# Kernel optimization log

Hardware: AMD Instinct MI355X
Metric: run time of the kernel (lower is better)

Reference implementation:

```python
import jax, jax.numpy as jnp
import numpy as np

N_HEAD = 16


def setup_inputs() -> dict:
    key = jax.random.key(0)
    ks = jax.random.split(key, 10)
    N, C, P = 4096, 2048, 8
    s = lambda k, shape, scale: jax.random.normal(k, shape, dtype=jnp.float32) * scale
    return {
        "x": s(ks[0], (N, C), 1.0),
        "rwkv_state": s(ks[1], (N, C), 1.0),
        "Wq": s(ks[2], (C, C), C ** -0.5),
        "Wk": s(ks[3], (C, C), C ** -0.5),
        "Wv": s(ks[4], (C, C), C ** -0.5),
        "Wo": s(ks[5], (C, C), 0.1 * C ** -0.5),
        "Wg": s(ks[6], (C, C), C ** -0.5),
        "bg": jnp.zeros((C,), dtype=jnp.float32),
        "Wb": s(ks[7], (2 * C, P * C), (2 * C) ** -0.5),
        "Wr": s(ks[8], (C, C), C ** -0.5),
    }


def reference(x, rwkv_state, Wq, Wk, Wv, Wo, Wg, bg, Wb, Wr):
    N, C = x.shape
    H = N_HEAD
    D = C // H
    # bridge: produce per-token tiny prefix [N, P, C] + reconstruction loss
    xs = jnp.concatenate([x, rwkv_state], axis=-1)      # [N, 2C]
    prefix = (xs @ Wb).reshape(N, -1, C)                # [N, P, C]
    recon = prefix.mean(axis=1) @ Wr                    # [N, C]
    recon_loss = jnp.mean((recon - x) ** 2)
    # per-token attention: query length 1 over P prefix keys
    q = (x @ Wq).reshape(N, H, D)                       # [N, H, D]
    k = (prefix @ Wk).reshape(N, -1, H, D)              # [N, P, H, D]
    v = (prefix @ Wv).reshape(N, -1, H, D)
    scores = jnp.einsum('nhd,nphd->nhp', q, k) / jnp.sqrt(jnp.float32(D))
    attn = jax.nn.softmax(scores, axis=-1)              # [N, H, P]
    out = jnp.einsum('nhp,nphd->nhd', attn, v).reshape(N, C)
    g = jax.nn.sigmoid(x @ Wg + bg)
    out = (out @ Wo) * g
    return out, recon_loss
```

## Files before the change

### kernel.cpp

```cpp
#include <hip/hip_runtime.h>

#define DEVFN static __device__ __forceinline__

typedef __attribute__((ext_vector_type(8))) short short8;
typedef __attribute__((ext_vector_type(4))) float f32x4;

DEVFN unsigned short f2bf(float f) {
    union { float f; unsigned u; } a; a.f = f;
    unsigned u = a.u;
    unsigned r = (u + 0x7FFFu + ((u >> 16) & 1u)) >> 16;
    return (unsigned short)r;
}
DEVFN float bf2f(unsigned short b) {
    union { unsigned u; float f; } a; a.u = ((unsigned)b) << 16;
    return a.f;
}
DEVFN float2 bfpair(unsigned v) {
    float2 r;
    union { unsigned u; float f; } a;
    a.u = (v & 0xFFFFu) << 16; r.x = a.f;
    a.u = v & 0xFFFF0000u;     r.y = a.f;
    return r;
}

DEVFN void gload16(const void* g, void* lds) {
    __builtin_amdgcn_global_load_lds(
        (const __attribute__((address_space(1))) unsigned int*)g,
        (__attribute__((address_space(3))) unsigned int*)lds, 16, 0, 0);
}

#define BAR() __builtin_amdgcn_s_barrier()
#define VMCNT8() asm volatile("s_waitcnt vmcnt(8)" ::: "memory")
#define VMCNT0() asm volatile("s_waitcnt vmcnt(0)" ::: "memory")

__global__ __launch_bounds__(256) void pack_xs_kernel(
        const float* __restrict__ x, const float* __restrict__ r,
        unsigned short* __restrict__ xs) {
    int i = blockIdx.x * 256 + threadIdx.x;
    int n  = i >> 10;
    int cw = i & 1023;
    const float* src = (cw < 512) ? (x + (size_t)n * 2048 + cw * 4)
                                  : (r + (size_t)n * 2048 + (cw - 512) * 4);
    float4 v = *(const float4*)src;
    ushort4 o;
    o.x = f2bf(v.x); o.y = f2bf(v.y); o.z = f2bf(v.z); o.w = f2bf(v.w);
    *(ushort4*)(xs + (size_t)n * 4096 + cw * 4) = o;
}

DEVFN void transpose_body(const float* __restrict__ in,
                          unsigned short* __restrict__ out,
                          int R, int Cc, int bx, int by) {
    __shared__ float tile[32][33];
    const int t  = threadIdx.x;
    const int r  = t >> 3;
    const int c4 = (t & 7) * 4;
    const int tr = by * 32, tc = bx * 32;
    float4 v = *(const float4*)(in + (size_t)(tr + r) * Cc + tc + c4);
    tile[r][c4 + 0] = v.x; tile[r][c4 + 1] = v.y;
    tile[r][c4 + 2] = v.z; tile[r][c4 + 3] = v.w;
    __syncthreads();
    const int orow = r, oc = c4;
    ushort4 o;
    o.x = f2bf(tile[oc + 0][orow]);
    o.y = f2bf(tile[oc + 1][orow]);
    o.z = f2bf(tile[oc + 2][orow]);
    o.w = f2bf(tile[oc + 3][orow]);
    *(ushort4*)(out + (size_t)(tc + orow) * R + tr + oc) = o;
}

__global__ __launch_bounds__(256) void transpose_cast_kernel(
        const float* __restrict__ in, unsigned short* __restrict__ out,
        int R, int Cc) {
    transpose_body(in, out, R, Cc, blockIdx.x, blockIdx.y);
}

__global__ __launch_bounds__(256) void transpose_cast6_kernel(
        const float* __restrict__ i0, const float* __restrict__ i1,
        const float* __restrict__ i2, const float* __restrict__ i3,
        const float* __restrict__ i4, const float* __restrict__ i5,
        unsigned short* __restrict__ o0, unsigned short* __restrict__ o1,
        unsigned short* __restrict__ o2, unsigned short* __restrict__ o3,
        unsigned short* __restrict__ o4, unsigned short* __restrict__ o5) {
    const float* in; unsigned short* out;
    switch (blockIdx.z) {
        case 0: in = i0; out = o0; break;
        case 1: in = i1; out = o1; break;
        case 2: in = i2; out = o2; break;
        case 3: in = i3; out = o3; break;
        case 4: in = i4; out = o4; break;
        default: in = i5; out = o5; break;
    }
    transpose_body(in, out, 2048, 2048, blockIdx.x, blockIdx.y);
}

template <int EPI>
__global__ __launch_bounds__(512, 2) void gemm256(
        const unsigned short* __restrict__ A, int lda,
        const unsigned short* __restrict__ Bt, int ldb,
        void* __restrict__ Cptr, void* __restrict__ Cptr2,
        int ldc, int splitcol, int K, int Mtiles,
        const float* __restrict__ aux_f32,
        const unsigned short* __restrict__ aux_bf16,
        float* __restrict__ loss_accum,
        const unsigned short* __restrict__ A2,
        const unsigned short* __restrict__ Bt2) {
    extern __shared__ char smem[];
    const int tid  = threadIdx.x;
    const int wid  = tid >> 6, lane = tid & 63;
    const int wm   = wid >> 2, wn = wid & 3;
    const int l15  = lane & 15;
    const int lhi  = (lane >> 4) * 16;
    const int nkt  = K >> 6;

    int bid = blockIdx.x;
    bool sub1 = false;
    if constexpr (EPI == 5) {
        const int half = gridDim.x >> 1;
        if (bid >= half) { sub1 = true; bid -= half; A = A2; Bt = Bt2; }
    }

    const int bandH = Mtiles >> 3;
    const int xcd = bid & 7, idx = bid >> 3;
    const int brow = (xcd * bandH + (idx % bandH)) << 8;
    const int bcol = (idx / bandH) << 8;

    const int lin0 = (wid * 2 + 0) * 1024 + lane * 16;
    const int lin1 = (wid * 2 + 1) * 1024 + lane * 16;
    const int ph0 = lin0 ^ (((lin0 >> 7) & 7) << 4);
    const int ph1v = lin1 ^ (((lin1 >> 7) & 7) << 4);
    const int srow0 = ph0 >> 7, scol0 = (ph0 & 127) >> 1;
    const int srow1 = ph1v >> 7, scol1 = (ph1v & 127) >> 1;
    const int dst0 = (wid * 2 + 0) * 1024;
    const int dst1 = (wid * 2 + 1) * 1024;

#define STAGE(t, mat, h) do { \
        char* base_ = smem + (((t) & 1) * 65536) + ((mat) * 32768) + ((h) * 16384); \
        const unsigned short* G_ = (mat) ? Bt : A; \
        const int ld_ = (mat) ? ldb : lda; \
        const int rb_ = ((mat) ? bcol : brow) + (h) * 128; \
        gload16(G_ + (size_t)(rb_ + srow0) * ld_ + (t) * 64 + scol0, base_ + dst0); \
        gload16(G_ + (size_t)(rb_ + srow1) * ld_ + (t) * 64 + scol1, base_ + dst1); \
    } while (0)
#define STAGE_G(t, mat, h) do { if ((t) < nkt) STAGE(t, mat, h); } while (0)

#define LDA_FRAG(dst, buf, m, kk) do { \
        int lin_ = ((m) * 16 + l15) * 128 + (kk) * 64 + lhi; \
        int ph_  = lin_ ^ (((lin_ >> 7) & 7) << 4); \
        dst = *(const short8*)(smem + (buf) * 65536 + wm * 16384 + ph_); \
    } while (0)
#define LDB_FRAG(dst, buf, n, kk) do { \
        int lin_ = ((wn & 1) * 64 + (n) * 16 + l15) * 128 + (kk) * 64 + lhi; \
        int ph_  = lin_ ^ (((lin_ >> 7) & 7) << 4); \
        dst = *(const short8*)(smem + (buf) * 65536 + 32768 + (wn >> 1) * 16384 + ph_); \
    } while (0)

    f32x4 acc[8][4] = {};
    short8 afr[8][2], bfr[4][2];

#define MFMA_Q(mq) do { \
        __builtin_amdgcn_s_setprio(1); \
        _Pragma("unroll") \
        for (int n_ = 0; n_ < 4; ++n_) { \
            acc[2*(mq)][n_]   = __builtin_amdgcn_mfma_f32_16x16x32_bf16(afr[2*(mq)][0],   bfr[n_][0], acc[2*(mq)][n_],   0,0,0); \
            acc[2*(mq)][n_]   = __builtin_amdgcn_mfma_f32_16x16x32_bf16(afr[2*(mq)][1],   bfr[n_][1], acc[2*(mq)][n_],   0,0,0); \
            acc[2*(mq)+1][n_] = __builtin_amdgcn_mfma_f32_16x16x32_bf16(afr[2*(mq)+1][0], bfr[n_][0], acc[2*(mq)+1][n_], 0,0,0); \
            acc[2*(mq)+1][n_] = __builtin_amdgcn_mfma_f32_16x16x32_bf16(afr[2*(mq)+1][1], bfr[n_][1], acc[2*(mq)+1][n_], 0,0,0); \
        } \
        __builtin_amdgcn_s_setprio(0); \
    } while (0)

#define READ_B(b) do { \
        _Pragma("unroll") \
        for (int n_ = 0; n_ < 4; ++n_) { LDB_FRAG(bfr[n_][0], b, n_, 0); LDB_FRAG(bfr[n_][1], b, n_, 1); } \
    } while (0)
#define READ_QA(b, mq) do { \
        LDA_FRAG(afr[2*(mq)][0],   b, 2*(mq),   0); LDA_FRAG(afr[2*(mq)][1],   b, 2*(mq),   1); \
        LDA_FRAG(afr[2*(mq)+1][0], b, 2*(mq)+1, 0); LDA_FRAG(afr[2*(mq)+1][1], b, 2*(mq)+1, 1); \
    } while (0)

    STAGE(0, 1, 0); STAGE(0, 1, 1); STAGE(0, 0, 0); STAGE(0, 0, 1);
    STAGE_G(1, 1, 0); STAGE_G(1, 1, 1); STAGE_G(1, 0, 0); STAGE_G(1, 0, 1);
    VMCNT8();
    BAR();

    const int niter = nkt >> 1;
    for (int it = 0; it < niter; ++it) {
        const int t0 = it * 2, t1 = t0 + 1;
        const bool lastIt = (it == niter - 1);

        READ_B(0); READ_QA(0, 0);
        BAR();
        MFMA_Q(0);
        READ_QA(0, 1);
        STAGE_G(t0 + 2, 1, 0);
        BAR();
        MFMA_Q(1);
        READ_QA(0, 2); READ_QA(0, 3);
        STAGE_G(t0 + 2, 1, 1);
        BAR();
        MFMA_Q(2);
        STAGE_G(t0 + 2, 0, 0); STAGE_G(t0 + 2, 0, 1);
        if (lastIt) { VMCNT0(); } else { VMCNT8(); }
        BAR();
        MFMA_Q(3);

        READ_B(1); READ_QA(1, 0);
        BAR();
        MFMA_Q(0);
        READ_QA(1, 1);
        STAGE_G(t1 + 2, 1, 0);
        BAR();
        MFMA_Q(1);
        READ_QA(1, 2); READ_QA(1, 3);
        STAGE_G(t1 + 2, 1, 1);
        BAR();
        MFMA_Q(2);
        STAGE_G(t1 + 2, 0, 0); STAGE_G(t1 + 2, 0, 1);
        if (lastIt) { VMCNT0(); } else { VMCNT8(); }
        BAR();
        MFMA_Q(3);
    }

    const int rl = (lane >> 4) * 4;
    const int cl = lane & 15;
    const int row0 = brow + wm * 128;

    if constexpr (EPI == 5) {
        const int col0 = bcol + wn * 64;
        if (!sub1) {
            float lsum = 0.f;
#pragma unroll
            for (int m = 0; m < 8; m++)
#pragma unroll
                for (int n = 0; n < 4; n++)
#pragma unroll
                    for (int rg = 0; rg < 4; rg++) {
                        int gr = row0 + m * 16 + rl + rg;
                        int gc = col0 + n * 16 + cl;
                        float d = acc[m][n][rg] - aux_f32[(size_t)gr * ldc + gc];
                        lsum += d * d;
                    }
#pragma unroll
            for (int msk = 1; msk < 64; msk <<= 1)
                lsum += __shfl_xor(lsum, msk, 64);
            if (lane == 0) atomicAdd(loss_accum, lsum);
        } else {
#pragma unroll
            for (int m = 0; m < 8; m++)
#pragma unroll
                for (int n = 0; n < 4; n++)
#pragma unroll
                    for (int rg = 0; rg < 4; rg++) {
                        int gr = row0 + m * 16 + rl + rg;
                        int gc = col0 + n * 16 + cl;
                        size_t idxo = (size_t)gr * ldc + gc;
                        float gv = bf2f(aux_bf16[idxo]);
                        ((float*)Cptr)[idxo] = acc[m][n][rg] * gv;
                    }
        }
        return;
    }

    void* Ceff = Cptr;
    bool second = false;
    int bcol_l = bcol;
    if constexpr (EPI == 0 || EPI == 4) {
        if (bcol >= splitcol) { Ceff = Cptr2; bcol_l = bcol - splitcol; second = true; }
    }
    const int col0 = bcol_l + wn * 64;

#pragma unroll
    for (int m = 0; m < 8; m++)
#pragma unroll
        for (int n = 0; n < 4; n++)
#pragma unroll
            for (int rg = 0; rg < 4; rg++) {
                int gr = row0 + m * 16 + rl + rg;
                int gc = col0 + n * 16 + cl;
                size_t idxo = (size_t)gr * ldc + gc;
                if constexpr (EPI == 0) {
                    ((unsigned short*)Ceff)[idxo] = f2bf(acc[m][n][rg]);
                } else {
                    if (second) {
                        float t = acc[m][n][rg] + aux_f32[gc];
                        ((unsigned short*)Ceff)[idxo] = f2bf(1.f / (1.f + expf(-t)));
                    } else {
                        ((unsigned short*)Ceff)[idxo] = f2bf(acc[m][n][rg]);
                    }
                }
            }
#undef STAGE
#undef STAGE_G
#undef LDA_FRAG
#undef LDB_FRAG
#undef MFMA_Q
#undef READ_B
#undef READ_QA
}

__global__ __launch_bounds__(256) void pmean_kernel(
        const unsigned short* __restrict__ prefix, unsigned short* __restrict__ pm) {
    int i  = blockIdx.x * 256 + threadIdx.x;
    int n  = i >> 8;
    int c8 = (i & 255) * 8;
    float acc[8] = {0, 0, 0, 0, 0, 0, 0, 0};
#pragma unroll
    for (int p = 0; p < 8; p++) {
        const unsigned short* src = prefix + (size_t)n * 16384 + p * 2048 + c8;
        uint4 raw = *(const uint4*)src;
        unsigned w[4] = {raw.x, raw.y, raw.z, raw.w};
#pragma unroll
        for (int j = 0; j < 4; j++) {
            float2 fp = bfpair(w[j]);
            acc[2 * j] += fp.x; acc[2 * j + 1] += fp.y;
        }
    }
    uint4 o;
    unsigned* ow = (unsigned*)&o;
#pragma unroll
    for (int j = 0; j < 4; j++)
        ow[j] = (unsigned)f2bf(acc[2 * j] * 0.125f) |
                ((unsigned)f2bf(acc[2 * j + 1] * 0.125f) << 16);
    *(uint4*)(pm + (size_t)n * 2048 + c8) = o;
}

__global__ __launch_bounds__(256) void attn_kernel(
        const unsigned short* __restrict__ q, const unsigned short* __restrict__ k,
        const unsigned short* __restrict__ v, unsigned short* __restrict__ o) {
    int gw   = (blockIdx.x * 256 + threadIdx.x) >> 6;
    int lane = threadIdx.x & 63;
    int n = gw >> 4, h = gw & 15;
    size_t qoff = (size_t)n * 2048 + h * 128 + lane * 2;
    float2 qv = bfpair(*(const unsigned*)(q + qoff));
    float s[8];
#pragma unroll
    for (int p = 0; p < 8; p++) {
        size_t koff = (size_t)(n * 8 + p) * 2048 + h * 128 + lane * 2;
        float2 kv = bfpair(*(const unsigned*)(k + koff));
        float d = qv.x * kv.x + qv.y * kv.y;
#pragma unroll
        for (int msk = 1; msk < 64; msk <<= 1) d += __shfl_xor(d, msk, 64);
        s[p] = d * 0.08838834764831845f;
    }
    float mx = s[0];
#pragma unroll
    for (int p = 1; p < 8; p++) mx = fmaxf(mx, s[p]);
    float e[8], den = 0.f;
#pragma unroll
    for (int p = 0; p < 8; p++) { e[p] = expf(s[p] - mx); den += e[p]; }
    float inv = 1.f / den;
    float o0 = 0.f, o1 = 0.f;
#pragma unroll
    for (int p = 0; p < 8; p++) {
        size_t voff = (size_t)(n * 8 + p) * 2048 + h * 128 + lane * 2;
        float2 vv = bfpair(*(const unsigned*)(v + voff));
        float a = e[p] * inv;
        o0 += a * vv.x; o1 += a * vv.y;
    }
    *(unsigned*)(o + qoff) = (unsigned)f2bf(o0) | ((unsigned)f2bf(o1) << 16);
}

__global__ __launch_bounds__(64) void finalize_loss_kernel(
        const float* __restrict__ accum, float* __restrict__ dst) {
    if (threadIdx.x == 0) dst[0] = accum[0] * (1.0f / (4096.0f * 2048.0f));
}

extern "C" void kernel_launch(void* const* d_in, const int* in_sizes, int n_in,
                              void* d_out, int out_size, void* d_ws, size_t ws_size,
                              hipStream_t stream) {
    const float* x    = (const float*)d_in[0];
    const float* rwkv = (const float*)d_in[1];
    const float* Wq   = (const float*)d_in[2];
    const float* Wk   = (const float*)d_in[3];
    const float* Wv   = (const float*)d_in[4];
    const float* Wo   = (const float*)d_in[5];
    const float* Wg   = (const float*)d_in[6];
    const float* bg   = (const float*)d_in[7];
    const float* Wb   = (const float*)d_in[8];
    const float* Wr   = (const float*)d_in[9];
    float* out = (float*)d_out;
    char*  ws  = (char*)d_ws;

    unsigned short* xs     = (unsigned short*)(ws + 0ull);
    unsigned short* wbT    = (unsigned short*)(ws + 33554432ull);
    unsigned short* wqT    = (unsigned short*)(ws + 167772160ull);
    unsigned short* wgT    = (unsigned short*)(ws + 176160768ull);
    unsigned short* wkT    = (unsigned short*)(ws + 184549376ull);
    unsigned short* wvT    = (unsigned short*)(ws + 192937984ull);
    unsigned short* wrT    = (unsigned short*)(ws + 201326592ull);
    unsigned short* woT    = (unsigned short*)(ws + 209715200ull);
    unsigned short* prefix = (unsigned short*)(ws + 218103808ull);
    unsigned short* vbuf   = (unsigned short*)(ws + 352321536ull);
    unsigned short* qbuf   = (unsigned short*)(ws + 486539264ull);
    unsigned short* gbuf   = (unsigned short*)(ws + 503316480ull);
    unsigned short* pmean  = (unsigned short*)(ws + 520093696ull);
    unsigned short* attno  = (unsigned short*)(ws + 536870912ull);
    float*          lossA  = (float*)(ws + 553648128ull);
    unsigned short* kbuf   = wbT;

    const int SMEM = 131072;
    const int BIG = 1 << 30;
    hipFuncSetAttribute(reinterpret_cast<const void*>(gemm256<0>),
                        hipFuncAttributeMaxDynamicSharedMemorySize, SMEM);
    hipFuncSetAttribute(reinterpret_cast<const void*>(gemm256<4>),
                        hipFuncAttributeMaxDynamicSharedMemorySize, SMEM);
    hipFuncSetAttribute(reinterpret_cast<const void*>(gemm256<5>),
                        hipFuncAttributeMaxDynamicSharedMemorySize, SMEM);

    hipMemsetAsync(lossA, 0, 16, stream);

    pack_xs_kernel<<<16384, 256, 0, stream>>>(x, rwkv, xs);
    transpose_cast_kernel<<<dim3(512, 128), 256, 0, stream>>>(Wb, wbT, 4096, 16384);
    transpose_cast6_kernel<<<dim3(64, 64, 6), 256, 0, stream>>>(
        Wq, Wg, Wk, Wv, Wr, Wo, wqT, wgT, wkT, wvT, wrT, woT);

    gemm256<0><<<dim3(1024), 512, SMEM, stream>>>(xs, 4096, wbT, 4096,
        prefix, nullptr, 16384, BIG, 4096, 16, nullptr, nullptr, nullptr,
        nullptr, nullptr);
    gemm256<0><<<dim3(2048), 512, SMEM, stream>>>(prefix, 2048, wkT, 2048,
        kbuf, vbuf, 2048, 2048, 2048, 128, nullptr, nullptr, nullptr,
        nullptr, nullptr);
    pmean_kernel<<<4096, 256, 0, stream>>>(prefix, pmean);
    gemm256<4><<<dim3(256), 512, SMEM, stream>>>(xs, 4096, wqT, 2048,
        qbuf, gbuf, 2048, 2048, 2048, 16, bg, nullptr, nullptr,
        nullptr, nullptr);
    attn_kernel<<<16384, 256, 0, stream>>>(qbuf, kbuf, vbuf, attno);
    gemm256<5><<<dim3(256), 512, SMEM, stream>>>(pmean, 2048, wrT, 2048,
        out, nullptr, 2048, BIG, 2048, 16, x, gbuf, lossA,
        attno, woT);

    finalize_loss_kernel<<<1, 64, 0, stream>>>(lossA, out + 8388608);
}
```

Baseline: 1.268 ms.

## Restructure GEMM main loop staging schedule and merge prep kernels into one launch

Merges the xs packing, Wb transpose-cast and six weight transpose-casts into a single prep kernel that dispatches on a flat block index, removing two launches. Reworks the GEMM main loop into two MFMA quarters per barrier, with fewer barriers per k-tile. The global-to-LDS staging order also changes: the A half of the next tile is issued later and the wait drops from vmcnt(8) to vmcnt(4). This cuts barrier overhead but shrinks the prefetch distance, which risks exposing more memory latency and raises correctness concerns around LDS buffer reuse.

After: 1.267 ms. No clear change (-0.1%).

```diff
diff --git a/kernel.cpp b/kernel.cpp
--- a/kernel.cpp
+++ b/kernel.cpp
@@ -30,13 +30,12 @@
 }
 
 #define BAR() __builtin_amdgcn_s_barrier()
-#define VMCNT8() asm volatile("s_waitcnt vmcnt(8)" ::: "memory")
+#define VMCNT4() asm volatile("s_waitcnt vmcnt(4)" ::: "memory")
 #define VMCNT0() asm volatile("s_waitcnt vmcnt(0)" ::: "memory")
 
-__global__ __launch_bounds__(256) void pack_xs_kernel(
-        const float* __restrict__ x, const float* __restrict__ r,
-        unsigned short* __restrict__ xs) {
-    int i = blockIdx.x * 256 + threadIdx.x;
+DEVFN void pack_xs_body(const float* __restrict__ x, const float* __restrict__ r,
+                        unsigned short* __restrict__ xs, int blk) {
+    int i = blk * 256 + threadIdx.x;
     int n  = i >> 10;
     int cw = i & 1023;
     const float* src = (cw < 512) ? (x + (size_t)n * 2048 + cw * 4)
@@ -68,21 +67,24 @@
     *(ushort4*)(out + (size_t)(tc + orow) * R + tr + oc) = o;
 }
 
-__global__ __launch_bounds__(256) void transpose_cast_kernel(
-        const float* __restrict__ in, unsigned short* __restrict__ out,
-        int R, int Cc) {
-    transpose_body(in, out, R, Cc, blockIdx.x, blockIdx.y);
-}
-
-__global__ __launch_bounds__(256) void transpose_cast6_kernel(
+__global__ __launch_bounds__(256) void prep_kernel(
+        const float* __restrict__ x, const float* __restrict__ rwkv,
+        unsigned short* __restrict__ xs,
+        const float* __restrict__ Wb, unsigned short* __restrict__ wbT,
         const float* __restrict__ i0, const float* __restrict__ i1,
         const float* __restrict__ i2, const float* __restrict__ i3,
         const float* __restrict__ i4, const float* __restrict__ i5,
         unsigned short* __restrict__ o0, unsigned short* __restrict__ o1,
         unsigned short* __restrict__ o2, unsigned short* __restrict__ o3,
         unsigned short* __restrict__ o4, unsigned short* __restrict__ o5) {
+    int b = blockIdx.x;
+    if (b < 16384) { pack_xs_body(x, rwkv, xs, b); return; }
+    b -= 16384;
+    if (b < 65536) { transpose_body(Wb, wbT, 4096, 16384, b & 511, b >> 9); return; }
+    b -= 65536;
+    const int z = b >> 12, rem = b & 4095;
     const float* in; unsigned short* out;
-    switch (blockIdx.z) {
+    switch (z) {
         case 0: in = i0; out = o0; break;
         case 1: in = i1; out = o1; break;
         case 2: in = i2; out = o2; break;
@@ -90,7 +92,7 @@
         case 4: in = i4; out = o4; break;
         default: in = i5; out = o5; break;
     }
-    transpose_body(in, out, 2048, 2048, blockIdx.x, blockIdx.y);
+    transpose_body(in, out, 2048, 2048, rem & 63, rem >> 6);
 }
 
 template <int EPI>
@@ -179,8 +181,8 @@
     } while (0)
 
     STAGE(0, 1, 0); STAGE(0, 1, 1); STAGE(0, 0, 0); STAGE(0, 0, 1);
-    STAGE_G(1, 1, 0); STAGE_G(1, 1, 1); STAGE_G(1, 0, 0); STAGE_G(1, 0, 1);
-    VMCNT8();
+    STAGE_G(1, 1, 0); STAGE_G(1, 1, 1);
+    VMCNT4();
     BAR();
 
     const int niter = nkt >> 1;
@@ -188,37 +190,24 @@
         const int t0 = it * 2, t1 = t0 + 1;
         const bool lastIt = (it == niter - 1);
 
-        READ_B(0); READ_QA(0, 0);
+        READ_B(0); READ_QA(0, 0); READ_QA(0, 1);
+        STAGE_G(t1, 0, 0); STAGE_G(t1, 0, 1);
         BAR();
-        MFMA_Q(0);
-        READ_QA(0, 1);
-        STAGE_G(t0 + 2, 1, 0);
+        MFMA_Q(0); MFMA_Q(1);
+        READ_QA(0, 2); READ_QA(0, 3);
+        STAGE_G(t0 + 2, 1, 0); STAGE_G(t0 + 2, 1, 1);
+        if (lastIt) { VMCNT0(); } else { VMCNT4(); }
         BAR();
-        MFMA_Q(1);
-        READ_QA(0, 2); READ_QA(0, 3);
-        STAGE_G(t0 + 2, 1, 1);
+        MFMA_Q(2); MFMA_Q(3);
+        READ_B(1); READ_QA(1, 0); READ_QA(1, 1);
+        STAGE_G(t0 + 2, 0, 0); STAGE_G(t0 + 2, 0, 1);
         BAR();
-        MFMA_Q(2);
-        STAGE_G(t0 + 2, 0, 0); STAGE_G(t0 + 2, 0, 1);
-        if (lastIt) { VMCNT0(); } else { VMCNT8(); }
+        MFMA_Q(0); MFMA_Q(1);
+        READ_QA(1, 2); READ_QA(1, 3);
+        STAGE_G(t1 + 2, 1, 0); STAGE_G(t1 + 2, 1, 1);
+        if (lastIt) { VMCNT0(); } else { VMCNT4(); }
         BAR();
-        MFMA_Q(3);
-
-        READ_B(1); READ_QA(1, 0);
-        BAR();
-        MFMA_Q(0);
-        READ_QA(1, 1);
-        STAGE_G(t1 + 2, 1, 0);
-        BAR();
-        MFMA_Q(1);
-        READ_QA(1, 2); READ_QA(1, 3);
-        STAGE_G(t1 + 2, 1, 1);
-        BAR();
-        MFMA_Q(2);
-        STAGE_G(t1 + 2, 0, 0); STAGE_G(t1 + 2, 0, 1);
-        if (lastIt) { VMCNT0(); } else { VMCNT8(); }
-        BAR();
-        MFMA_Q(3);
+        MFMA_Q(2); MFMA_Q(3);
     }
 
     const int rl = (lane >> 4) * 4;
@@ -409,9 +398,8 @@
 
     hipMemsetAsync(lossA, 0, 16, stream);
 
-    pack_xs_kernel<<<16384, 256, 0, stream>>>(x, rwkv, xs);
-    transpose_cast_kernel<<<dim3(512, 128), 256, 0, stream>>>(Wb, wbT, 4096, 16384);
-    transpose_cast6_kernel<<<dim3(64, 64, 6), 256, 0, stream>>>(
+    prep_kernel<<<106496, 256, 0, stream>>>(
+        x, rwkv, xs, Wb, wbT,
         Wq, Wg, Wk, Wv, Wr, Wo, wqT, wgT, wkT, wvT, wrT, woT);
 
     gemm256<0><<<dim3(1024), 512, SMEM, stream>>>(xs, 4096, wbT, 4096,
```
